# Performance work log

Hardware: AMD Instinct MI355X
Metric: run time of the kernel (lower is better)

The kernel has to match this reference:

```python
import jax, jax.numpy as jnp
import numpy as np

D_MODEL, D_INNER, D_STATE, DT_RANK, K = 768, 1536, 16, 48, 4
B, L = 2, 1024


def causal_depthwise_conv(x, w, b):
    # x: [B, L, D], w: [D, 1, K], b: [D]; torch pads K-1 both sides then slices [:L] -> causal left pad
    xt = x.transpose(0, 2, 1)  # [B, D, L]
    out = jax.lax.conv_general_dilated(
        xt, w, window_strides=(1,), padding=[(K - 1, 0)],
        dimension_numbers=('NCH', 'OIH', 'NCH'), feature_group_count=xt.shape[1])
    return out.transpose(0, 2, 1) + b


def ssm(xc, A_log, D, W_dt, dtW, dtb, W_B, W_C):
    # xc: [B, L, Din]
    A = -jnp.exp(A_log)                                   # [Din, N]
    dt_low = jnp.einsum('bld,rd->blr', xc, W_dt)          # [B, L, R]
    delta = jax.nn.softplus(jnp.einsum('blr,dr->bld', dt_low, dtW) + dtb)  # [B, L, Din]
    Bm = jnp.einsum('bld,nd->bln', xc, W_B)               # [B, L, N]
    Cm = jnp.einsum('bld,nd->bln', xc, W_C)               # [B, L, N]
    deltaA = jnp.exp(delta[..., None] * A)                # [B, L, Din, N]
    BX = (delta * xc)[..., None] * Bm[:, :, None, :]      # [B, L, Din, N]

    def combine(e1, e2):
        a1, b1 = e1
        a2, b2 = e2
        return a1 * a2, a2 * b1 + b2

    _, hs = jax.lax.associative_scan(combine, (deltaA, BX), axis=1)  # [B, L, Din, N]
    y = jnp.einsum('bldn,bln->bld', hs, Cm) + D * xc
    return y


def setup_inputs() -> dict:
    key = jax.random.key(0)
    ks = jax.random.split(key, 20)
    s = 0.02
    A_init = jnp.log(jnp.broadcast_to(jnp.arange(1, D_STATE + 1, dtype=jnp.float32), (D_INNER, D_STATE)))
    return {
        'x': jax.random.normal(ks[0], (B, L, D_MODEL), jnp.float32),
        'W_in_states': jax.random.normal(ks[1], (D_INNER, D_MODEL), jnp.float32) * s,
        'W_in_gates': jax.random.normal(ks[2], (D_INNER, D_MODEL), jnp.float32) * s,
        'conv_w': jax.random.normal(ks[3], (D_INNER, 1, K), jnp.float32) * 0.2,
        'conv_b': jax.random.normal(ks[4], (D_INNER,), jnp.float32) * 0.02,
        'conv_w_b': jax.random.normal(ks[5], (D_INNER, 1, K), jnp.float32) * 0.2,
        'conv_b_b': jax.random.normal(ks[6], (D_INNER,), jnp.float32) * 0.02,
        'W_dt': jax.random.normal(ks[7], (DT_RANK, D_INNER), jnp.float32) * s,
        'W_B': jax.random.normal(ks[8], (D_STATE, D_INNER), jnp.float32) * s,
        'W_C': jax.random.normal(ks[9], (D_STATE, D_INNER), jnp.float32) * s,
        'dtW': jax.random.normal(ks[10], (D_INNER, DT_RANK), jnp.float32) * s,
        'dtb': jax.random.normal(ks[11], (D_INNER,), jnp.float32) * 0.1,
        'A_log': A_init,
        'Dp': jnp.ones((D_INNER,), jnp.float32),
        'W_dt_b': jax.random.normal(ks[12], (DT_RANK, D_INNER), jnp.float32) * s,
        'W_B_b': jax.random.normal(ks[13], (D_STATE, D_INNER), jnp.float32) * s,
        'W_C_b': jax.random.normal(ks[14], (D_STATE, D_INNER), jnp.float32) * s,
        'dtW_b': jax.random.normal(ks[15], (D_INNER, DT_RANK), jnp.float32) * s,
        'dtb_b': jax.random.normal(ks[16], (D_INNER,), jnp.float32) * 0.1,
        'A_log_b': A_init,
        'Dp_b': jnp.ones((D_INNER,), jnp.float32),
        'W_out': jax.random.normal(ks[17], (D_MODEL, D_INNER), jnp.float32) * s,
    }


def reference(x, W_in_states, W_in_gates, conv_w, conv_b, conv_w_b, conv_b_b,
              W_dt, W_B, W_C, dtW, dtb, A_log, Dp,
              W_dt_b, W_B_b, W_C_b, dtW_b, dtb_b, A_log_b, Dp_b, W_out):
    xs = jnp.einsum('blm,dm->bld', x, W_in_states)  # [B, L, Din]
    z = jnp.einsum('blm,dm->bld', x, W_in_gates)    # [B, L, Din]
    # forward branch
    xc = jax.nn.silu(causal_depthwise_conv(xs, conv_w, conv_b))
    y = ssm(xc, A_log, Dp, W_dt, dtW, dtb, W_B, W_C)
    # backward branch: xz flipped along L, split -> reversed xs / reversed z
    xs_b = xs[:, ::-1]
    z_b = z[:, ::-1]
    xcb = jax.nn.silu(causal_depthwise_conv(xs_b, conv_w_b, conv_b_b))
    y_b = ssm(xcb, A_log_b, Dp_b, W_dt_b, dtW_b, dtb_b, W_B_b, W_C_b)
    # gating
    y = y * jax.nn.silu(z)
    y_b = y_b * jax.nn.silu(z_b)
    y = (y + y_b[:, ::-1]) * 0.5  # divide_output
    return jnp.einsum('bld,md->blm', y, W_out)
```

## Files before the change

### kernel.cpp

```cpp
#include <hip/hip_runtime.h>
#include <hip/hip_bf16.h>
#include <stdint.h>

#define DM 768
#define DI 1536
#define DSTATE 16
#define RNK 48
#define BB 2
#define LL 1024
#define ML (BB * LL)

#define NSEG 32
#define SEGL (LL / NSEG)

typedef unsigned short u16;
typedef __bf16 bf16x8 __attribute__((ext_vector_type(8)));
typedef float f32x4 __attribute__((ext_vector_type(4)));

struct __align__(8) u16x4_t { u16 x, y, z, w; };

__device__ __forceinline__ float b2f(u16 u) {
  union { uint32_t i; float f; } v; v.i = ((uint32_t)u) << 16; return v.f;
}
__device__ __forceinline__ u16 f2b(float f) {
  union { float f; uint32_t i; } v; v.f = f;
  uint32_t r = v.i + 0x7FFFu + ((v.i >> 16) & 1u);
  return (u16)(r >> 16);
}
__device__ __forceinline__ float silu_f(float x) { return x / (1.f + __expf(-x)); }
__device__ __forceinline__ float softplus_f(float s) {
  return fmaxf(s, 0.f) + __logf(1.f + __expf(-fabsf(s)));
}
__device__ __forceinline__ u16x4_t cvt4(float4 v) {
  u16x4_t o; o.x = f2b(v.x); o.y = f2b(v.y); o.z = f2b(v.z); o.w = f2b(v.w); return o;
}

__device__ __forceinline__ void gl16(const u16* g, u16* l) {
  __builtin_amdgcn_global_load_lds(
      (const __attribute__((address_space(1))) uint32_t*)g,
      (__attribute__((address_space(3))) uint32_t*)l, 16, 0, 0);
}

#define SEG_X    (ML * DM / 4)
#define SEG_W    (DI * DM / 4)
#define SEG_CAT  (128 * DI / 4)
#define SEG_DTW  (DI * 64 / 4)
__global__ __launch_bounds__(256) void convert_kernel(
    const float4* __restrict__ x, const float4* __restrict__ wis,
    const float4* __restrict__ wig, const float4* __restrict__ wout,
    const float* __restrict__ W_B, const float* __restrict__ W_C,
    const float* __restrict__ W_dt,
    const float* __restrict__ W_B_b, const float* __restrict__ W_C_b,
    const float* __restrict__ W_dt_b,
    const float* __restrict__ dtW, const float* __restrict__ dtW_b,
    u16x4_t* __restrict__ xb, u16x4_t* __restrict__ wisb,
    u16x4_t* __restrict__ wigb, u16x4_t* __restrict__ woutb,
    u16x4_t* __restrict__ wcf, u16x4_t* __restrict__ wcb,
    u16x4_t* __restrict__ dtwf, u16x4_t* __restrict__ dtwb)
{
  int idx = blockIdx.x * 256 + threadIdx.x;
  if (idx < SEG_X) { xb[idx] = cvt4(x[idx]); return; }
  idx -= SEG_X;
  if (idx < SEG_W) { wisb[idx] = cvt4(wis[idx]); return; }
  idx -= SEG_W;
  if (idx < SEG_W) { wigb[idx] = cvt4(wig[idx]); return; }
  idx -= SEG_W;
  if (idx < SEG_W) { woutb[idx] = cvt4(wout[idx]); return; }
  idx -= SEG_W;
  if (idx < 2 * SEG_CAT) {
    int dir = idx / SEG_CAT;
    int rem = idx % SEG_CAT;
    int row = rem / (DI / 4), k4 = rem % (DI / 4);
    const float* src = nullptr;
    if (row < 16)      src = (dir ? W_B_b  : W_B)  + (size_t)row * DI + k4 * 4;
    else if (row < 32) src = (dir ? W_C_b  : W_C)  + (size_t)(row - 16) * DI + k4 * 4;
    else if (row < 80) src = (dir ? W_dt_b : W_dt) + (size_t)(row - 32) * DI + k4 * 4;
    u16x4_t o;
    if (src) o = cvt4(*(const float4*)src);
    else { o.x = 0; o.y = 0; o.z = 0; o.w = 0; }
    (dir ? wcb : wcf)[rem] = o;
    return;
  }
  idx -= 2 * SEG_CAT;
  int dir = idx / SEG_DTW;
  int rem = idx % SEG_DTW;
  int d = rem / 16, r4 = rem % 16;
  const float* Dw = dir ? dtW_b : dtW;
  u16x4_t o;
  if (r4 < 12) o = cvt4(*(const float4*)(Dw + (size_t)d * RNK + r4 * 4));
  else { o.x = 0; o.y = 0; o.z = 0; o.w = 0; }
  (dir ? dtwb : dtwf)[rem] = o;
}

__global__ __launch_bounds__(256) void gemm_bt(
    const u16* __restrict__ A, const u16* __restrict__ B0,
    const u16* __restrict__ B1, int Nsplit,
    void* __restrict__ Cout, int M, int N, int K, int ldc, int epi,
    const u16* __restrict__ A2, const u16* __restrict__ B2,
    void* __restrict__ C2,
    u16* __restrict__ Caux, u16* __restrict__ Caux2,
    const float* __restrict__ ebias, const float* __restrict__ ebias2)
{
  if (blockIdx.z) { A = A2; B0 = B2; Cout = C2; Caux = Caux2; ebias = ebias2; }
  __shared__ alignas(16) u16 As[2][128 * 32];
  __shared__ alignas(16) u16 Bs[2][128 * 32];
  const int tid = threadIdx.x;
  const int wave = tid >> 6, lane = tid & 63;
  const int bm = blockIdx.y * 128;
  const int bn = blockIdx.x * 128;

  const u16* Bmat = B0;
  int ncol0 = bn;
  int epi_l = epi;
  if (B1 != nullptr && bn >= Nsplit) { Bmat = B1; ncol0 = bn - Nsplit; epi_l = 1; }

  const int c0 = tid, c1 = tid + 256;
  const u16* gA0 = A + (size_t)(bm + (c0 >> 2)) * K + (c0 & 3) * 8;
  const u16* gA1 = A + (size_t)(bm + (c1 >> 2)) * K + (c1 & 3) * 8;
  const u16* gB0 = Bmat + (size_t)(ncol0 + (c0 >> 2)) * K + (c0 & 3) * 8;
  const u16* gB1 = Bmat + (size_t)(ncol0 + (c1 >> 2)) * K + (c1 & 3) * 8;

  const int wm = (wave & 1) * 64, wn = (wave >> 1) * 64;
  const int rl = lane & 15, q = lane >> 4;

  f32x4 acc[4][4];
#pragma unroll
  for (int i = 0; i < 4; ++i)
#pragma unroll
    for (int j = 0; j < 4; ++j) acc[i][j] = (f32x4){0.f, 0.f, 0.f, 0.f};

  auto stage = [&](int buf, int k0) {
    gl16(gA0 + k0, &As[buf][c0 * 8]);
    gl16(gA1 + k0, &As[buf][c1 * 8]);
    gl16(gB0 + k0, &Bs[buf][c0 * 8]);
    gl16(gB1 + k0, &Bs[buf][c1 * 8]);
  };

  stage(0, 0);
  __syncthreads();
  int cur = 0;
  for (int k0 = 0; k0 < K; k0 += 32) {
    const bool more = (k0 + 32 < K);
    if (more) stage(cur ^ 1, k0 + 32);

    const bf16x8* AsV = (const bf16x8*)As[cur];
    const bf16x8* BsV = (const bf16x8*)Bs[cur];
    bf16x8 af[4], bfv[4];
#pragma unroll
    for (int s = 0; s < 4; ++s) {
      af[s]  = AsV[(wm + s * 16 + rl) * 4 + q];
      bfv[s] = BsV[(wn + s * 16 + rl) * 4 + q];
    }
#pragma unroll
    for (int i = 0; i < 4; ++i)
#pragma unroll
      for (int j = 0; j < 4; ++j)
        acc[i][j] = __builtin_amdgcn_mfma_f32_16x16x32_bf16(af[i], bfv[j], acc[i][j], 0, 0, 0);

    if (more) {
      __syncthreads();
      cur ^= 1;
    }
  }

#pragma unroll
  for (int i = 0; i < 4; ++i) {
#pragma unroll
    for (int j = 0; j < 4; ++j) {
#pragma unroll
      for (int r = 0; r < 4; ++r) {
        int row = bm + wm + i * 16 + q * 4 + r;
        int col = bn + wn + j * 16 + rl;
        float v = acc[i][j][r];
        if (epi_l == 1) v = silu_f(v);
        if (epi == 5) {
          if (col < 32)      ((float*)Cout)[(size_t)row * 32 + col] = v;
          else if (col < 96) Caux[(size_t)row * 64 + (col - 32)] = f2b(v);
        } else if (epi == 6) {
          ((u16*)Cout)[(size_t)row * ldc + col] = f2b(softplus_f(v + ebias[col]));
        } else if (epi == 2) {
          ((float*)Cout)[(size_t)row * ldc + col] = v;
        } else {
          ((u16*)Cout)[(size_t)row * ldc + col] = f2b(v);
        }
      }
    }
  }
}

__global__ __launch_bounds__(256) void gemm_out64(
    const u16* __restrict__ A, const u16* __restrict__ Bw,
    float* __restrict__ out)
{
  __shared__ alignas(16) u16 As[64 * 72];
  __shared__ alignas(16) u16 Bs[64 * 72];
  const int tid = threadIdx.x;
  const int wave = tid >> 6, lane = tid & 63;
  const int bm = blockIdx.y * 64;
  const int bn = blockIdx.x * 64;

  const int c0 = tid, c1 = tid + 256;
  const u16* gA0 = A + (size_t)(bm + (c0 >> 3)) * DI + (c0 & 7) * 8;
  const u16* gA1 = A + (size_t)(bm + (c1 >> 3)) * DI + (c1 & 7) * 8;
  const u16* gB0 = Bw + (size_t)(bn + (c0 >> 3)) * DI + (c0 & 7) * 8;
  const u16* gB1 = Bw + (size_t)(bn + (c1 >> 3)) * DI + (c1 & 7) * 8;
  uint4* lA0 = (uint4*)&As[(c0 >> 3) * 72 + (c0 & 7) * 8];
  uint4* lA1 = (uint4*)&As[(c1 >> 3) * 72 + (c1 & 7) * 8];
  uint4* lB0 = (uint4*)&Bs[(c0 >> 3) * 72 + (c0 & 7) * 8];
  uint4* lB1 = (uint4*)&Bs[(c1 >> 3) * 72 + (c1 & 7) * 8];

  const int rl = lane & 15, q = lane >> 4;

  f32x4 acc[4];
#pragma unroll
  for (int s = 0; s < 4; ++s) acc[s] = (f32x4){0.f, 0.f, 0.f, 0.f};

  uint4 ra0 = *(const uint4*)gA0, ra1 = *(const uint4*)gA1;
  uint4 rb0 = *(const uint4*)gB0, rb1 = *(const uint4*)gB1;

  for (int k0 = 0; k0 < DI; k0 += 64) {
    *lA0 = ra0; *lA1 = ra1; *lB0 = rb0; *lB1 = rb1;
    __syncthreads();
    if (k0 + 64 < DI) {
      ra0 = *(const uint4*)(gA0 + k0 + 64);
      ra1 = *(const uint4*)(gA1 + k0 + 64);
      rb0 = *(const uint4*)(gB0 + k0 + 64);
      rb1 = *(const uint4*)(gB1 + k0 + 64);
    }
    bf16x8 bf[2], af;
#pragma unroll
    for (int c = 0; c < 2; ++c)
      bf[c] = *(const bf16x8*)&Bs[(wave * 16 + rl) * 72 + c * 32 + q * 8];
#pragma unroll
    for (int s = 0; s < 4; ++s) {
#pragma unroll
      for (int c = 0; c < 2; ++c) {
        af = *(const bf16x8*)&As[(s * 16 + rl) * 72 + c * 32 + q * 8];
        acc[s] = __builtin_amdgcn_mfma_f32_16x16x32_bf16(af, bf[c], acc[s], 0, 0, 0);
      }
    }
    __syncthreads();
  }

#pragma unroll
  for (int s = 0; s < 4; ++s) {
#pragma unroll
    for (int r = 0; r < 4; ++r) {
      int row = bm + s * 16 + q * 4 + r;
      int col = bn + wave * 16 + rl;
      out[(size_t)row * DM + col] = acc[s][r];
    }
  }
}

__global__ void conv_kernel(
    const u16* __restrict__ xsg,
    const float* __restrict__ cw, const float* __restrict__ cb,
    const float* __restrict__ cwb, const float* __restrict__ cbb,
    u16* __restrict__ xc, u16* __restrict__ xcb)
{
  int idx = blockIdx.x * 256 + threadIdx.x;
  int d = idx % DI;
  int row = idx / DI;
  int l = row % LL, b = row / LL;
  const u16* base = xsg + (size_t)b * LL * 3072 + d;

  float4 wf = *(const float4*)(cw + d * 4);
  float4 wb = *(const float4*)(cwb + d * 4);
  float wfk[4] = {wf.x, wf.y, wf.z, wf.w};
  float wbk[4] = {wb.x, wb.y, wb.z, wb.w};

  float accf = cb[d];
  float accb = cbb[d];
#pragma unroll
  for (int k = 0; k < 4; ++k) {
    int ls = l - 3 + k;
    if (ls >= 0) {
      accf += wfk[k] * b2f(base[(size_t)ls * 3072]);
      accb += wbk[k] * b2f(base[(size_t)(LL - 1 - ls) * 3072]);
    }
  }
  xc[idx]  = f2b(silu_f(accf));
  xcb[idx] = f2b(silu_f(accb));
}

__global__ void combine_kernel(
    const u16* __restrict__ ybr, const u16* __restrict__ xsg, u16* yf)
{
  int idx = blockIdx.x * 256 + threadIdx.x;
  int d = idx % DI;
  int row = idx / DI;
  int l = row % LL, b = row / LL;
  float g = b2f(xsg[(size_t)row * 3072 + DI + d]);
  float vb = b2f(ybr[((size_t)b * LL + (LL - 1 - l)) * DI + d]);
  float v = 0.5f * (b2f(yf[idx]) + vb) * g;
  yf[idx] = f2b(v);
}

__global__ __launch_bounds__(256) void scan_sum(
    const u16* __restrict__ df, const u16* __restrict__ db,
    const u16* __restrict__ xcf, const u16* __restrict__ xcb,
    const float* __restrict__ pf, const float* __restrict__ pb,
    const float* __restrict__ A_log, const float* __restrict__ A_log_b,
    float* __restrict__ sdl, float* __restrict__ bs)
{
  const int dir = blockIdx.z / NSEG, seg = blockIdx.z % NSEG;
  const u16* delta = dir ? db : df;
  const u16* xc = dir ? xcb : xcf;
  const float* proj = dir ? pb : pf;
  const float* Al = dir ? A_log_b : A_log;
  const int b = blockIdx.y;
  const int d = blockIdx.x * 256 + threadIdx.x;
  const int l0 = seg * SEGL;

  __shared__ float Bsh[SEGL][16];
  for (int i = threadIdx.x; i < SEGL * 16; i += 256) {
    int l = i >> 4, n = i & 15;
    Bsh[l][n] = proj[((size_t)b * LL + l0 + l) * 32 + n];
  }
  __syncthreads();

  float An[16];
#pragma unroll
  for (int n = 0; n < 16; ++n) An[n] = -__expf(Al[d * 16 + n]);

  float h[16];
#pragma unroll
  for (int n = 0; n < 16; ++n) h[n] = 0.f;
  float S = 0.f;

  const u16* dbase = delta + ((size_t)b * LL + l0) * DI + d;
  const u16* xbase = xc + ((size_t)b * LL + l0) * DI + d;

  for (int g = 0; g < SEGL; g += 4) {
    float dl4[4], dx4[4];
#pragma unroll
    for (int j = 0; j < 4; ++j) {
      float dv = b2f(dbase[(size_t)(g + j) * DI]);
      float xv = b2f(xbase[(size_t)(g + j) * DI]);
      dl4[j] = dv; dx4[j] = dv * xv;
    }
#pragma unroll
    for (int j = 0; j < 4; ++j) {
      S += dl4[j];
#pragma unroll
      for (int n = 0; n < 16; ++n)
        h[n] = __expf(dl4[j] * An[n]) * h[n] + dx4[j] * Bsh[g + j][n];
    }
  }

  size_t base = (((size_t)dir * BB + b) * NSEG + seg) * DI + d;
  sdl[base] = S;
#pragma unroll
  for (int n = 0; n < 16; ++n) bs[base * 16 + n] = h[n];
}

__global__ __launch_bounds__(256) void scan_carry(
    const float* __restrict__ A_log, const float* __restrict__ A_log_b,
    const float* __restrict__ sdl, float* __restrict__ bs)
{
  int idx = blockIdx.x * 256 + threadIdx.x;
  int n = idx & 15;
  int t = idx >> 4;
  int d = t % DI;
  int b = (t / DI) % BB;
  int dir = t / (DI * BB);
  const float* Al = dir ? A_log_b : A_log;
  float An = -__expf(Al[d * 16 + n]);
  float h = 0.f;
  for (int s = 0; s < NSEG; ++s) {
    size_t base = (((size_t)dir * BB + b) * NSEG + s) * DI + d;
    float S = sdl[base];
    float bv = bs[base * 16 + n];
    bs[base * 16 + n] = h;
    h = __expf(S * An) * h + bv;
  }
}

__global__ __launch_bounds__(256) void scan_apply(
    const u16* __restrict__ df, const u16* __restrict__ db,
    const u16* __restrict__ xcf, const u16* __restrict__ xcb,
    const float* __restrict__ pf, const float* __restrict__ pb,
    const float* __restrict__ A_log, const float* __restrict__ A_log_b,
    const float* __restrict__ Dp, const float* __restrict__ Dp_b,
    const float* __restrict__ bs,
    u16* __restrict__ y_f, u16* __restrict__ y_b)
{
  const int dir = blockIdx.z / NSEG, seg = blockIdx.z % NSEG;
  const u16* delta = dir ? db : df;
  const u16* xc = dir ? xcb : xcf;
  const float* proj = dir ? pb : pf;
  const float* Al = dir ? A_log_b : A_log;
  const float* Dpp = dir ? Dp_b : Dp;
  u16* y = dir ? y_b : y_f;
  const int b = blockIdx.y;
  const int d = blockIdx.x * 256 + threadIdx.x;
  const int l0 = seg * SEGL;

  __shared__ float BCsh[SEGL][32];
  for (int i = threadIdx.x; i < SEGL * 32; i += 256) {
    int l = i >> 5, j = i & 31;
    BCsh[l][j] = proj[((size_t)b * LL + l0 + l) * 32 + j];
  }
  __syncthreads();

  float An[16];
#pragma unroll
  for (int n = 0; n < 16; ++n) An[n] = -__expf(Al[d * 16 + n]);
  const float Dv = Dpp[d];

  float h[16];
  size_t cbase = (((size_t)dir * BB + b) * NSEG + seg) * DI + d;
#pragma unroll
  for (int n = 0; n < 16; ++n) h[n] = bs[cbase * 16 + n];

  const u16* dbase = delta + ((size_t)b * LL + l0) * DI + d;
  const u16* xbase = xc + ((size_t)b * LL + l0) * DI + d;
  u16* ybase = y + ((size_t)b * LL + l0) * DI + d;

  for (int g = 0; g < SEGL; g += 4) {
    float dl4[4], xv4[4];
#pragma unroll
    for (int j = 0; j < 4; ++j) {
      dl4[j] = b2f(dbase[(size_t)(g + j) * DI]);
      xv4[j] = b2f(xbase[(size_t)(g + j) * DI]);
    }
#pragma unroll
    for (int j = 0; j < 4; ++j) {
      float dx = dl4[j] * xv4[j];
      float yv = 0.f;
#pragma unroll
      for (int n = 0; n < 16; ++n) {
        h[n] = __expf(dl4[j] * An[n]) * h[n] + dx * BCsh[g + j][n];
        yv += h[n] * BCsh[g + j][16 + n];
      }
      ybase[(size_t)(g + j) * DI] = f2b(yv + Dv * xv4[j]);
    }
  }
}

extern "C" void kernel_launch(void* const* d_in, const int* in_sizes, int n_in,
                              void* d_out, int out_size, void* d_ws, size_t ws_size,
                              hipStream_t stream)
{
  const float* x       = (const float*)d_in[0];
  const float* Wis     = (const float*)d_in[1];
  const float* Wig     = (const float*)d_in[2];
  const float* conv_w  = (const float*)d_in[3];
  const float* conv_b  = (const float*)d_in[4];
  const float* conv_wb = (const float*)d_in[5];
  const float* conv_bb = (const float*)d_in[6];
  const float* W_dt    = (const float*)d_in[7];
  const float* W_B     = (const float*)d_in[8];
  const float* W_C     = (const float*)d_in[9];
  const float* dtW     = (const float*)d_in[10];
  const float* dtb     = (const float*)d_in[11];
  const float* A_log   = (const float*)d_in[12];
  const float* Dp      = (const float*)d_in[13];
  const float* W_dt_b  = (const float*)d_in[14];
  const float* W_B_b   = (const float*)d_in[15];
  const float* W_C_b   = (const float*)d_in[16];
  const float* dtW_b   = (const float*)d_in[17];
  const float* dtb_b   = (const float*)d_in[18];
  const float* A_log_b = (const float*)d_in[19];
  const float* Dp_b    = (const float*)d_in[20];
  const float* W_out   = (const float*)d_in[21];

  char* ws = (char*)d_ws;
  size_t off = 0;
  auto alloc = [&](size_t bytes) -> char* {
    char* p = ws + off; off += (bytes + 255) & ~(size_t)255; return p;
  };
  u16*   xb    = (u16*)alloc((size_t)ML * DM * 2);
  u16*   wisb  = (u16*)alloc((size_t)DI * DM * 2);
  u16*   wigb  = (u16*)alloc((size_t)DI * DM * 2);
  u16*   woutb = (u16*)alloc((size_t)DM * DI * 2);
  u16*   xsg = (u16*)alloc((size_t)ML * 3072 * 2);
  u16*   xc  = (u16*)alloc((size_t)ML * DI * 2);
  u16*   xcb = (u16*)alloc((size_t)ML * DI * 2);
  u16*   wcf = (u16*)alloc((size_t)128 * DI * 2);
  u16*   wcb = (u16*)alloc((size_t)128 * DI * 2);
  u16*   dtwf = (u16*)alloc((size_t)DI * 64 * 2);
  u16*   dtwb = (u16*)alloc((size_t)DI * 64 * 2);
  float* pf  = (float*)alloc((size_t)ML * 32 * 4);
  float* pb  = (float*)alloc((size_t)ML * 32 * 4);
  u16*   dtlf = (u16*)alloc((size_t)ML * 64 * 2);
  u16*   dtlb = (u16*)alloc((size_t)ML * 64 * 2);
  u16*   df  = (u16*)alloc((size_t)ML * DI * 2);
  u16*   db  = (u16*)alloc((size_t)ML * DI * 2);
  u16*   yf  = (u16*)alloc((size_t)ML * DI * 2);
  u16*   ybr = (u16*)alloc((size_t)ML * DI * 2);
  float* sdl = (float*)alloc((size_t)2 * BB * NSEG * DI * 4);
  float* bs  = (float*)alloc((size_t)2 * BB * NSEG * DI * 16 * 4);

  const int conv_total = SEG_X + 3 * SEG_W + 2 * SEG_CAT + 2 * SEG_DTW;
  convert_kernel<<<(conv_total + 255) / 256, 256, 0, stream>>>(
      (const float4*)x, (const float4*)Wis, (const float4*)Wig, (const float4*)W_out,
      W_B, W_C, W_dt, W_B_b, W_C_b, W_dt_b, dtW, dtW_b,
      (u16x4_t*)xb, (u16x4_t*)wisb, (u16x4_t*)wigb, (u16x4_t*)woutb,
      (u16x4_t*)wcf, (u16x4_t*)wcb, (u16x4_t*)dtwf, (u16x4_t*)dtwb);

  gemm_bt<<<dim3(3072 / 128, ML / 128, 1), 256, 0, stream>>>(
      xb, wisb, wigb, DI, xsg, ML, 3072, DM, 3072, 0,
      nullptr, nullptr, nullptr, nullptr, nullptr, nullptr, nullptr);

  conv_kernel<<<(ML * DI) / 256, 256, 0, stream>>>(
      xsg, conv_w, conv_b, conv_wb, conv_bb, xc, xcb);

  gemm_bt<<<dim3(1, ML / 128, 2), 256, 0, stream>>>(
      xc, wcf, nullptr, 1 << 30, pf, ML, 128, DI, 32, 5,
      xcb, wcb, pb, dtlf, dtlb, nullptr, nullptr);

  gemm_bt<<<dim3(DI / 128, ML / 128, 2), 256, 0, stream>>>(
      dtlf, dtwf, nullptr, 1 << 30, df, ML, DI, 64, DI, 6,
      dtlb, dtwb, db, nullptr, nullptr, dtb, dtb_b);

  scan_sum<<<dim3(DI / 256, BB, 2 * NSEG), 256, 0, stream>>>(
      df, db, xc, xcb, pf, pb, A_log, A_log_b, sdl, bs);
  scan_carry<<<(2 * BB * DI * 16) / 256, 256, 0, stream>>>(
      A_log, A_log_b, sdl, bs);
  scan_apply<<<dim3(DI / 256, BB, 2 * NSEG), 256, 0, stream>>>(
      df, db, xc, xcb, pf, pb, A_log, A_log_b, Dp, Dp_b, bs, yf, ybr);

  combine_kernel<<<(ML * DI) / 256, 256, 0, stream>>>(ybr, xsg, yf);

  gemm_out64<<<dim3(DM / 64, ML / 64, 1), 256, 0, stream>>>(
      yf, woutb, (float*)d_out);
}
```

Baseline: 305.5 us.

## Split-K the x_proj GEMM with partial-sum buffer and reduction kernel

The x_proj GEMM (xc times the concatenated B/C/dt_low weights, N=128, K=1536) previously launched only 32 blocks, which leaves most CUs idle. It now splits K into 8 chunks so 256 blocks each write fp32 partials to a scratch buffer. A new reduction kernel sums the partials and writes the B/C fp32 and dt_low bf16 outputs. The cost is an extra launch and about 16 MB of partial-sum traffic, and the special epilogue modes are removed from gemm_bt.

Measured after the change: 265.6 us. -13.1%, faster.

```diff
diff --git a/kernel.cpp b/kernel.cpp
--- a/kernel.cpp
+++ b/kernel.cpp
@@ -12,6 +12,9 @@
 
 #define NSEG 32
 #define SEGL (LL / NSEG)
+
+#define PROJ_NCHUNK 8
+#define PROJ_KC (DI / PROJ_NCHUNK)
 
 typedef unsigned short u16;
 typedef __bf16 bf16x8 __attribute__((ext_vector_type(8)));
@@ -98,10 +101,9 @@
     void* __restrict__ Cout, int M, int N, int K, int ldc, int epi,
     const u16* __restrict__ A2, const u16* __restrict__ B2,
     void* __restrict__ C2,
-    u16* __restrict__ Caux, u16* __restrict__ Caux2,
     const float* __restrict__ ebias, const float* __restrict__ ebias2)
 {
-  if (blockIdx.z) { A = A2; B0 = B2; Cout = C2; Caux = Caux2; ebias = ebias2; }
+  if (blockIdx.z) { A = A2; B0 = B2; Cout = C2; ebias = ebias2; }
   __shared__ alignas(16) u16 As[2][128 * 32];
   __shared__ alignas(16) u16 Bs[2][128 * 32];
   const int tid = threadIdx.x;
@@ -173,19 +175,112 @@
         int col = bn + wn + j * 16 + rl;
         float v = acc[i][j][r];
         if (epi_l == 1) v = silu_f(v);
-        if (epi == 5) {
-          if (col < 32)      ((float*)Cout)[(size_t)row * 32 + col] = v;
-          else if (col < 96) Caux[(size_t)row * 64 + (col - 32)] = f2b(v);
-        } else if (epi == 6) {
+        if (epi == 6) {
           ((u16*)Cout)[(size_t)row * ldc + col] = f2b(softplus_f(v + ebias[col]));
-        } else if (epi == 2) {
-          ((float*)Cout)[(size_t)row * ldc + col] = v;
         } else {
           ((u16*)Cout)[(size_t)row * ldc + col] = f2b(v);
         }
       }
     }
   }
+}
+
+__global__ __launch_bounds__(256) void gemm_proj_sk(
+    const u16* __restrict__ xcf, const u16* __restrict__ xcb,
+    const u16* __restrict__ wcf, const u16* __restrict__ wcb,
+    float* __restrict__ part)
+{
+  const int dir = blockIdx.z;
+  const u16* A = dir ? xcb : xcf;
+  const u16* B = dir ? wcb : wcf;
+  const int kc = blockIdx.x;
+  const int bm = blockIdx.y * 128;
+  const int kbase = kc * PROJ_KC;
+
+  __shared__ alignas(16) u16 As[128 * 32];
+  __shared__ alignas(16) u16 Bs[128 * 32];
+  const int tid = threadIdx.x;
+  const int wave = tid >> 6, lane = tid & 63;
+  const int c0 = tid, c1 = tid + 256;
+  const u16* gA0 = A + (size_t)(bm + (c0 >> 2)) * DI + kbase + (c0 & 3) * 8;
+  const u16* gA1 = A + (size_t)(bm + (c1 >> 2)) * DI + kbase + (c1 & 3) * 8;
+  const u16* gB0 = B + (size_t)(c0 >> 2) * DI + kbase + (c0 & 3) * 8;
+  const u16* gB1 = B + (size_t)(c1 >> 2) * DI + kbase + (c1 & 3) * 8;
+  uint4* lA0 = (uint4*)&As[c0 * 8]; uint4* lA1 = (uint4*)&As[c1 * 8];
+  uint4* lB0 = (uint4*)&Bs[c0 * 8]; uint4* lB1 = (uint4*)&Bs[c1 * 8];
+
+  const int wm = (wave & 1) * 64, wn = (wave >> 1) * 64;
+  const int rl = lane & 15, q = lane >> 4;
+
+  f32x4 acc[4][4];
+#pragma unroll
+  for (int i = 0; i < 4; ++i)
+#pragma unroll
+    for (int j = 0; j < 4; ++j) acc[i][j] = (f32x4){0.f, 0.f, 0.f, 0.f};
+
+  const bf16x8* AsV = (const bf16x8*)As;
+  const bf16x8* BsV = (const bf16x8*)Bs;
+
+  uint4 ra0 = *(const uint4*)(gA0);
+  uint4 ra1 = *(const uint4*)(gA1);
+  uint4 rb0 = *(const uint4*)(gB0);
+  uint4 rb1 = *(const uint4*)(gB1);
+
+  for (int k0 = 0; k0 < PROJ_KC; k0 += 32) {
+    *lA0 = ra0; *lA1 = ra1; *lB0 = rb0; *lB1 = rb1;
+    __syncthreads();
+    if (k0 + 32 < PROJ_KC) {
+      ra0 = *(const uint4*)(gA0 + k0 + 32);
+      ra1 = *(const uint4*)(gA1 + k0 + 32);
+      rb0 = *(const uint4*)(gB0 + k0 + 32);
+      rb1 = *(const uint4*)(gB1 + k0 + 32);
+    }
+    bf16x8 af[4], bfv[4];
+#pragma unroll
+    for (int s = 0; s < 4; ++s) {
+      af[s]  = AsV[(wm + s * 16 + rl) * 4 + q];
+      bfv[s] = BsV[(wn + s * 16 + rl) * 4 + q];
+    }
+#pragma unroll
+    for (int i = 0; i < 4; ++i)
+#pragma unroll
+      for (int j = 0; j < 4; ++j)
+        acc[i][j] = __builtin_amdgcn_mfma_f32_16x16x32_bf16(af[i], bfv[j], acc[i][j], 0, 0, 0);
+    __syncthreads();
+  }
+
+  float* pout = part + ((size_t)(dir * PROJ_NCHUNK + kc) * ML + bm) * 128;
+#pragma unroll
+  for (int i = 0; i < 4; ++i) {
+#pragma unroll
+    for (int j = 0; j < 4; ++j) {
+#pragma unroll
+      for (int r = 0; r < 4; ++r) {
+        int row = wm + i * 16 + q * 4 + r;
+        int col = wn + j * 16 + rl;
+        pout[(size_t)row * 128 + col] = acc[i][j][r];
+      }
+    }
+  }
+}
+
+__global__ __launch_bounds__(256) void proj_reduce(
+    const float* __restrict__ part,
+    float* __restrict__ pf, float* __restrict__ pb,
+    u16* __restrict__ dtlf, u16* __restrict__ dtlb)
+{
+  int idx = blockIdx.x * 256 + threadIdx.x;
+  int col = idx % 96;
+  int t = idx / 96;
+  int row = t % ML;
+  int dir = t / ML;
+  const float* p = part + ((size_t)dir * PROJ_NCHUNK * ML + row) * 128 + col;
+  float s = 0.f;
+#pragma unroll
+  for (int c = 0; c < PROJ_NCHUNK; ++c)
+    s += p[(size_t)c * ML * 128];
+  if (col < 32) (dir ? pb : pf)[(size_t)row * 32 + col] = s;
+  else          (dir ? dtlb : dtlf)[(size_t)row * 64 + (col - 32)] = f2b(s);
 }
 
 __global__ __launch_bounds__(256) void gemm_out64(
@@ -492,6 +587,7 @@
   u16*   ybr = (u16*)alloc((size_t)ML * DI * 2);
   float* sdl = (float*)alloc((size_t)2 * BB * NSEG * DI * 4);
   float* bs  = (float*)alloc((size_t)2 * BB * NSEG * DI * 16 * 4);
+  float* part = (float*)alloc((size_t)2 * PROJ_NCHUNK * ML * 128 * 4);
 
   const int conv_total = SEG_X + 3 * SEG_W + 2 * SEG_CAT + 2 * SEG_DTW;
   convert_kernel<<<(conv_total + 255) / 256, 256, 0, stream>>>(
@@ -502,18 +598,19 @@
 
   gemm_bt<<<dim3(3072 / 128, ML / 128, 1), 256, 0, stream>>>(
       xb, wisb, wigb, DI, xsg, ML, 3072, DM, 3072, 0,
-      nullptr, nullptr, nullptr, nullptr, nullptr, nullptr, nullptr);
+      nullptr, nullptr, nullptr, nullptr, nullptr);
 
   conv_kernel<<<(ML * DI) / 256, 256, 0, stream>>>(
       xsg, conv_w, conv_b, conv_wb, conv_bb, xc, xcb);
 
-  gemm_bt<<<dim3(1, ML / 128, 2), 256, 0, stream>>>(
-      xc, wcf, nullptr, 1 << 30, pf, ML, 128, DI, 32, 5,
-      xcb, wcb, pb, dtlf, dtlb, nullptr, nullptr);
+  gemm_proj_sk<<<dim3(PROJ_NCHUNK, ML / 128, 2), 256, 0, stream>>>(
+      xc, xcb, wcf, wcb, part);
+  proj_reduce<<<(2 * ML * 96) / 256, 256, 0, stream>>>(
+      part, pf, pb, dtlf, dtlb);
 
   gemm_bt<<<dim3(DI / 128, ML / 128, 2), 256, 0, stream>>>(
       dtlf, dtwf, nullptr, 1 << 30, df, ML, DI, 64, DI, 6,
-      dtlb, dtwb, db, nullptr, nullptr, dtb, dtb_b);
+      dtlb, dtwb, db, dtb, dtb_b);
 
   scan_sum<<<dim3(DI / 256, BB, 2 * NSEG), 256, 0, stream>>>(
       df, db, xc, xcb, pf, pb, A_log, A_log_b, sdl, bs);
```
